# Optimization experiments

Measured on AMD Instinct MI355X. Metric: run time of the kernel, lower is better.

Reference implementation:

```python
import jax, jax.numpy as jnp
import numpy as np

EMB_DIM = 1024
N_HEADS = 16
HEAD_DIM = EMB_DIM // N_HEADS


def setup_inputs() -> dict:
    key = jax.random.key(0)
    ks = jax.random.split(key, 6)
    B, T, C = 2, 2048, EMB_DIM
    s = 1.0 / np.sqrt(C)
    return {
        "x": jax.random.normal(ks[0], (B, T, C), dtype=jnp.float32),
        "W_query": jax.random.normal(ks[1], (C, C), dtype=jnp.float32) * s,
        "W_key": jax.random.normal(ks[2], (C, C), dtype=jnp.float32) * s,
        "W_value": jax.random.normal(ks[3], (C, C), dtype=jnp.float32) * s,
        "W_out": jax.random.normal(ks[4], (C, C), dtype=jnp.float32) * s,
        "b_out": jax.random.normal(ks[5], (C,), dtype=jnp.float32) * 0.01,
    }


def reference(x, W_query, W_key, W_value, W_out, b_out):
    # x: [B, T, C]. Linear weights stored as [in, out] (transposed torch layout).
    B, T, C = x.shape
    H, D = N_HEADS, HEAD_DIM

    def split_heads(t):  # [B,T,C] -> [B,H,T,D]
        return t.reshape(B, T, H, D).transpose(0, 2, 1, 3)

    q = split_heads(x @ W_query)
    k = split_heads(x @ W_key)
    v = split_heads(x @ W_value)

    scale = 1.0 / jnp.sqrt(jnp.asarray(D, dtype=x.dtype))
    att = jnp.einsum("bhqd,bhkd->bhqk", q, k) * scale  # [B,H,T,T]
    causal = jnp.tril(jnp.ones((T, T), dtype=bool))
    att = jnp.where(causal[None, None], att, jnp.asarray(-jnp.inf, dtype=att.dtype))
    att = jax.nn.softmax(att, axis=-1)
    # dropout is identity in eval / drop_rate=0
    y = jnp.einsum("bhqk,bhkd->bhqd", att, v)  # [B,H,T,D]
    y = y.transpose(0, 2, 1, 3).reshape(B, T, C)
    return y @ W_out + b_out
```

## Files before the change

### kernel.cpp

```cpp
#include <hip/hip_runtime.h>
#include <hip/hip_bf16.h>
#include <math.h>

#define Bsz 2
#define Tsz 2048
#define Csz 1024
#define Hsz 16
#define Dsz 64

typedef __attribute__((ext_vector_type(8))) short frag8;
typedef __attribute__((ext_vector_type(4))) float f4;
typedef __attribute__((ext_vector_type(8))) unsigned short us8;

static __device__ __forceinline__ unsigned short f2bf(float f) {
  union { __hip_bfloat16 h; unsigned short u; } c;
  c.h = __float2bfloat16(f);
  return c.u;
}

#define GLDS16(g, l)                                                        \
  __builtin_amdgcn_global_load_lds(                                         \
      (const __attribute__((address_space(1))) void*)(g),                   \
      (__attribute__((address_space(3))) void*)(l), 16, 0, 0)

__global__ __launch_bounds__(256) void cast_x(const float* __restrict__ x,
                                              unsigned short* __restrict__ xb) {
  const int i = (blockIdx.x * 256 + threadIdx.x) * 8;
  const float4 a = *(const float4*)(x + i);
  const float4 b = *(const float4*)(x + i + 4);
  us8 v;
  v[0] = f2bf(a.x); v[1] = f2bf(a.y); v[2] = f2bf(a.z); v[3] = f2bf(a.w);
  v[4] = f2bf(b.x); v[5] = f2bf(b.y); v[6] = f2bf(b.z); v[7] = f2bf(b.w);
  *(us8*)(xb + i) = v;
}

__global__ __launch_bounds__(256) void transpose_cast(
    const float* __restrict__ s0, const float* __restrict__ s1,
    const float* __restrict__ s2, const float* __restrict__ s3,
    unsigned short* __restrict__ d0, unsigned short* __restrict__ d1,
    unsigned short* __restrict__ d2, unsigned short* __restrict__ d3) {
  __shared__ float Ls[64][65];
  const int mat = blockIdx.x >> 8;
  const int tile = blockIdx.x & 255;
  const float* src = mat == 0 ? s0 : mat == 1 ? s1 : mat == 2 ? s2 : s3;
  unsigned short* dst = mat == 0 ? d0 : mat == 1 ? d1 : mat == 2 ? d2 : d3;
  const int tr0 = (tile >> 4) << 6, tc0 = (tile & 15) << 6;
  const int t = threadIdx.x;
  const int lr = t >> 4, lc = (t & 15) << 2;
#pragma unroll
  for (int j = 0; j < 4; ++j) {
    const float4 v = *(const float4*)(src + (size_t)(tr0 + lr + j * 16) * 1024 + tc0 + lc);
    Ls[lr + j * 16][lc + 0] = v.x;
    Ls[lr + j * 16][lc + 1] = v.y;
    Ls[lr + j * 16][lc + 2] = v.z;
    Ls[lr + j * 16][lc + 3] = v.w;
  }
  __syncthreads();
#pragma unroll
  for (int j = 0; j < 4; ++j) {
    ushort4 v;
    v.x = f2bf(Ls[lc + 0][lr + j * 16]);
    v.y = f2bf(Ls[lc + 1][lr + j * 16]);
    v.z = f2bf(Ls[lc + 2][lr + j * 16]);
    v.w = f2bf(Ls[lc + 3][lr + j * 16]);
    *(ushort4*)(dst + (size_t)(tc0 + lr + j * 16) * 1024 + tr0 + lc) = v;
  }
}

template <int MODE>
__global__ __launch_bounds__(256) void mm_bt(
    const unsigned short* __restrict__ A, const unsigned short* __restrict__ Bt,
    const float* __restrict__ bias, unsigned short* __restrict__ O0,
    unsigned short* __restrict__ O1, float* __restrict__ Of) {
  __shared__ __align__(16) unsigned short As[128 * 32];
  __shared__ __align__(16) unsigned short Bs[128 * 32];
  const int K = 1024;
  const int tid = threadIdx.x;
  const int wave = tid >> 6, lane = tid & 63;
  const int quad = lane >> 4, l16 = lane & 15;
  const int wm = wave >> 1, wn = wave & 1;
  const int row0 = blockIdx.y << 7, col0 = blockIdx.x << 7;

  const int sr = lane >> 2, sg = lane & 3;
  const int rA0 = wave * 32 + sr;
  const int g0 = sg ^ ((rA0 >> 1) & 3);
  const unsigned short* gA0 = A + (size_t)(row0 + rA0) * K + (g0 << 3);
  const unsigned short* gA1 = gA0 + (size_t)16 * K;
  const unsigned short* gB0 = Bt + (size_t)(col0 + rA0) * K + (g0 << 3);
  const unsigned short* gB1 = gB0 + (size_t)16 * K;
  unsigned short* lA0 = &As[(wave * 32) * 32];
  unsigned short* lA1 = &As[(wave * 32 + 16) * 32];
  unsigned short* lB0 = &Bs[(wave * 32) * 32];
  unsigned short* lB1 = &Bs[(wave * 32 + 16) * 32];

  f4 acc[4][4];
#pragma unroll
  for (int i = 0; i < 4; ++i)
#pragma unroll
    for (int j = 0; j < 4; ++j) acc[i][j] = (f4){0.f, 0.f, 0.f, 0.f};

  for (int kk = 0; kk < K; kk += 32) {
    __syncthreads();
    GLDS16(gA0 + kk, lA0);
    GLDS16(gA1 + kk, lA1);
    GLDS16(gB0 + kk, lB0);
    GLDS16(gB1 + kk, lB1);
    __syncthreads();

    frag8 af[4], bf[4];
#pragma unroll
    for (int mt = 0; mt < 4; ++mt) {
      const int r = wm * 64 + mt * 16 + l16;
      af[mt] = *(const frag8*)&As[r * 32 + ((quad ^ ((r >> 1) & 3)) << 3)];
    }
#pragma unroll
    for (int nt = 0; nt < 4; ++nt) {
      const int n = wn * 64 + nt * 16 + l16;
      bf[nt] = *(const frag8*)&Bs[n * 32 + ((quad ^ ((n >> 1) & 3)) << 3)];
    }
#pragma unroll
    for (int mt = 0; mt < 4; ++mt)
#pragma unroll
      for (int nt = 0; nt < 4; ++nt)
        acc[mt][nt] = __builtin_amdgcn_mfma_f32_16x16x32_bf16(af[mt], bf[nt], acc[mt][nt], 0, 0, 0);
  }

  if (MODE == 0) {
    const bool isK = (col0 >= 1024);
    unsigned short* dst = isK ? O1 : O0;
    const float sc = isK ? 1.0f : 0.125f;
#pragma unroll
    for (int mt = 0; mt < 4; ++mt)
#pragma unroll
      for (int nt = 0; nt < 4; ++nt) {
        const int m = row0 + wm * 64 + mt * 16 + quad * 4;
        const int n = (col0 & 1023) + wn * 64 + nt * 16 + l16;
        const int b = m >> 11, h = n >> 6, d = n & 63;
#pragma unroll
        for (int r = 0; r < 4; ++r) {
          const int tk = (m + r) & (Tsz - 1);
          dst[(((size_t)b * Hsz + h) * Tsz + tk) * Dsz + d] = f2bf(acc[mt][nt][r] * sc);
        }
      }
  } else if (MODE == 1) {
#pragma unroll
    for (int mt = 0; mt < 4; ++mt)
#pragma unroll
      for (int nt = 0; nt < 4; ++nt) {
        const int ch = row0 + wm * 64 + mt * 16 + quad * 4;
        const int tok = col0 + wn * 64 + nt * 16 + l16;
        const int b = tok >> 11, tk = tok & (Tsz - 1);
#pragma unroll
        for (int r = 0; r < 4; ++r) {
          const int h = (ch + r) >> 6, d = (ch + r) & 63;
          O0[(((size_t)b * Hsz + h) * Dsz + d) * Tsz + tk] = f2bf(acc[mt][nt][r]);
        }
      }
  } else {
#pragma unroll
    for (int mt = 0; mt < 4; ++mt)
#pragma unroll
      for (int nt = 0; nt < 4; ++nt) {
        const int m = row0 + wm * 64 + mt * 16 + quad * 4;
        const int n = col0 + wn * 64 + nt * 16 + l16;
        const float bv = bias[n];
#pragma unroll
        for (int r = 0; r < 4; ++r)
          Of[(size_t)(m + r) * Csz + n] = acc[mt][nt][r] + bv;
      }
  }
}

#define PST 40
__global__ __launch_bounds__(256) void attn_mfma(
    const unsigned short* __restrict__ Qb,
    const unsigned short* __restrict__ Kb,
    const unsigned short* __restrict__ VTb,
    unsigned short* __restrict__ Y) {
  __shared__ __align__(16) unsigned short Pbuf[4][32 * PST];
  const int wave = threadIdx.x >> 6;
  const int lane = threadIdx.x & 63;
  const int quad = lane >> 4;
  const int l16 = lane & 15;

  const int bh = blockIdx.x >> 4;
  int qt = blockIdx.x & 15;
  if (bh >= 16) qt = 15 - qt;

  const int qbase = qt * 128 + wave * 32;

  const unsigned short* Qh = Qb + (size_t)bh * Tsz * Dsz;
  const unsigned short* Kh = Kb + (size_t)bh * Tsz * Dsz;
  const unsigned short* Vh = VTb + (size_t)bh * Dsz * Tsz;

  frag8 qf[2][2];
#pragma unroll
  for (int m = 0; m < 2; ++m)
#pragma unroll
    for (int ks = 0; ks < 2; ++ks)
      qf[m][ks] = *(const frag8*)(Qh + (size_t)(qbase + m * 16 + l16) * Dsz + ks * 32 + quad * 8);

  f4 o[2][4];
  float lsum[2][4];
#pragma unroll
  for (int m = 0; m < 2; ++m) {
#pragma unroll
    for (int nt = 0; nt < 4; ++nt) o[m][nt] = (f4){0.f, 0.f, 0.f, 0.f};
#pragma unroll
    for (int r = 0; r < 4; ++r) lsum[m][r] = 0.f;
  }

  unsigned short* Pw = &Pbuf[wave][0];
  const f4 zf = (f4){0.f, 0.f, 0.f, 0.f};

  const int kend = qbase + 32;
  for (int k0 = 0; k0 < kend; k0 += 32) {
    frag8 kf[2][2];
#pragma unroll
    for (int n = 0; n < 2; ++n)
#pragma unroll
      for (int ks = 0; ks < 2; ++ks)
        kf[n][ks] = *(const frag8*)(Kh + (size_t)(k0 + n * 16 + l16) * Dsz + ks * 32 + quad * 8);
    frag8 vf[4];
#pragma unroll
    for (int nt = 0; nt < 4; ++nt)
      vf[nt] = *(const frag8*)(Vh + (size_t)(nt * 16 + l16) * Tsz + k0 + quad * 8);

    f4 s[2][2];
#pragma unroll
    for (int m = 0; m < 2; ++m)
#pragma unroll
      for (int n = 0; n < 2; ++n) {
        f4 a = __builtin_amdgcn_mfma_f32_16x16x32_bf16(qf[m][0], kf[n][0], zf, 0, 0, 0);
        s[m][n] = __builtin_amdgcn_mfma_f32_16x16x32_bf16(qf[m][1], kf[n][1], a, 0, 0, 0);
      }

#pragma unroll
    for (int m = 0; m < 2; ++m) {
      const int qr0 = qbase + m * 16 + quad * 4;
#pragma unroll
      for (int n = 0; n < 2; ++n) {
        const int kc = k0 + n * 16 + l16;
#pragma unroll
        for (int r = 0; r < 4; ++r) {
          const float sv = (kc <= qr0 + r) ? s[m][n][r] : -INFINITY;
          const float p = __expf(sv);
          lsum[m][r] += p;
          Pw[(m * 16 + quad * 4 + r) * PST + n * 16 + l16] = f2bf(p);
        }
      }
    }

    frag8 pf[2];
#pragma unroll
    for (int m = 0; m < 2; ++m)
      pf[m] = *(const frag8*)(&Pw[(m * 16 + l16) * PST + quad * 8]);

#pragma unroll
    for (int m = 0; m < 2; ++m)
#pragma unroll
      for (int nt = 0; nt < 4; ++nt)
        o[m][nt] = __builtin_amdgcn_mfma_f32_16x16x32_bf16(pf[m], vf[nt], o[m][nt], 0, 0, 0);
  }

#pragma unroll
  for (int off = 1; off < 16; off <<= 1)
#pragma unroll
    for (int m = 0; m < 2; ++m)
#pragma unroll
      for (int r = 0; r < 4; ++r)
        lsum[m][r] += __shfl_xor(lsum[m][r], off);

  const int b = bh >> 4, h = bh & 15;
#pragma unroll
  for (int m = 0; m < 2; ++m) {
#pragma unroll
    for (int r = 0; r < 4; ++r) {
      const float inv = 1.f / lsum[m][r];
      const int trow = qbase + m * 16 + quad * 4 + r;
      unsigned short* yp = Y + ((size_t)b * Tsz + trow) * Csz + h * 64 + l16;
#pragma unroll
      for (int nt = 0; nt < 4; ++nt)
        yp[nt * 16] = f2bf(o[m][nt][r] * inv);
    }
  }
}

extern "C" void kernel_launch(void* const* d_in, const int* in_sizes, int n_in,
                              void* d_out, int out_size, void* d_ws, size_t ws_size,
                              hipStream_t stream) {
  const float* x  = (const float*)d_in[0];
  const float* Wq = (const float*)d_in[1];
  const float* Wk = (const float*)d_in[2];
  const float* Wv = (const float*)d_in[3];
  const float* Wo = (const float*)d_in[4];
  const float* bo = (const float*)d_in[5];

  const size_t NTOK = (size_t)Bsz * Tsz;
  const size_t NEL = NTOK * Csz;
  unsigned short* xb   = (unsigned short*)d_ws;
  unsigned short* WqkT = xb + NEL;
  unsigned short* WvT  = WqkT + 2 * Csz * Csz;
  unsigned short* WoT  = WvT + Csz * Csz;
  unsigned short* Qb   = WoT + Csz * Csz;
  unsigned short* Kb   = Qb + NEL;
  unsigned short* VTb  = Kb + NEL;
  unsigned short* Yb   = VTb + NEL;

  cast_x<<<NEL / 2048, 256, 0, stream>>>(x, xb);
  transpose_cast<<<1024, 256, 0, stream>>>(Wq, Wk, Wv, Wo,
                                           WqkT, WqkT + Csz * Csz, WvT, WoT);

  mm_bt<0><<<dim3(16, 32), 256, 0, stream>>>(xb, WqkT, nullptr, Qb, Kb, nullptr);
  mm_bt<1><<<dim3(32, 8), 256, 0, stream>>>(WvT, xb, nullptr, VTb, nullptr, nullptr);

  attn_mfma<<<Bsz * Hsz * (Tsz / 128), 256, 0, stream>>>(Qb, Kb, VTb, Yb);

  mm_bt<2><<<dim3(8, 32), 256, 0, stream>>>(Yb, WoT, bo, nullptr, nullptr, (float*)d_out);
}
```

Measured before the change: 220.4 us.

## Fuse QKV projection into one GEMM and stage K/V tiles through LDS in attention

The V projection now runs inside the Q/K GEMM launch as a third column range, and writes transposed V with vectorized stores, which removes one kernel launch. The attention kernel now uses 64-query blocks with 16 queries per wave. All four waves share K and V chunks that are double-buffered into swizzled LDS via global_load_lds, instead of each wave reading them from global memory separately. The change also transposes the QK^T MFMA, skips masking on chunks that lie fully below the diagonal, and raises launch_bounds occupancy. In exchange it adds block-wide syncs per chunk and smaller per-wave tiles.

```diff
diff --git a/kernel.cpp b/kernel.cpp
--- a/kernel.cpp
+++ b/kernel.cpp
@@ -71,7 +71,8 @@
 __global__ __launch_bounds__(256) void mm_bt(
     const unsigned short* __restrict__ A, const unsigned short* __restrict__ Bt,
     const float* __restrict__ bias, unsigned short* __restrict__ O0,
-    unsigned short* __restrict__ O1, float* __restrict__ Of) {
+    unsigned short* __restrict__ O1, unsigned short* __restrict__ O2,
+    float* __restrict__ Of) {
   __shared__ __align__(16) unsigned short As[128 * 32];
   __shared__ __align__(16) unsigned short Bs[128 * 32];
   const int K = 1024;
@@ -126,36 +127,38 @@
   }
 
   if (MODE == 0) {
-    const bool isK = (col0 >= 1024);
-    unsigned short* dst = isK ? O1 : O0;
-    const float sc = isK ? 1.0f : 0.125f;
-#pragma unroll
-    for (int mt = 0; mt < 4; ++mt)
-#pragma unroll
-      for (int nt = 0; nt < 4; ++nt) {
-        const int m = row0 + wm * 64 + mt * 16 + quad * 4;
-        const int n = (col0 & 1023) + wn * 64 + nt * 16 + l16;
-        const int b = m >> 11, h = n >> 6, d = n & 63;
-#pragma unroll
-        for (int r = 0; r < 4; ++r) {
-          const int tk = (m + r) & (Tsz - 1);
-          dst[(((size_t)b * Hsz + h) * Tsz + tk) * Dsz + d] = f2bf(acc[mt][nt][r] * sc);
-        }
-      }
-  } else if (MODE == 1) {
-#pragma unroll
-    for (int mt = 0; mt < 4; ++mt)
-#pragma unroll
-      for (int nt = 0; nt < 4; ++nt) {
-        const int ch = row0 + wm * 64 + mt * 16 + quad * 4;
-        const int tok = col0 + wn * 64 + nt * 16 + l16;
-        const int b = tok >> 11, tk = tok & (Tsz - 1);
-#pragma unroll
-        for (int r = 0; r < 4; ++r) {
-          const int h = (ch + r) >> 6, d = (ch + r) & 63;
-          O0[(((size_t)b * Hsz + h) * Dsz + d) * Tsz + tk] = f2bf(acc[mt][nt][r]);
-        }
-      }
+    if (col0 < 2048) {
+      const bool isK = (col0 >= 1024);
+      unsigned short* dst = isK ? O1 : O0;
+      const float sc = isK ? 1.0f : 0.125f;
+#pragma unroll
+      for (int mt = 0; mt < 4; ++mt)
+#pragma unroll
+        for (int nt = 0; nt < 4; ++nt) {
+          const int m = row0 + wm * 64 + mt * 16 + quad * 4;
+          const int n = (col0 & 1023) + wn * 64 + nt * 16 + l16;
+          const int b = m >> 11, h = n >> 6, d = n & 63;
+#pragma unroll
+          for (int r = 0; r < 4; ++r) {
+            const int tk = (m + r) & (Tsz - 1);
+            dst[(((size_t)b * Hsz + h) * Tsz + tk) * Dsz + d] = f2bf(acc[mt][nt][r] * sc);
+          }
+        }
+    } else {
+#pragma unroll
+      for (int mt = 0; mt < 4; ++mt)
+#pragma unroll
+        for (int nt = 0; nt < 4; ++nt) {
+          const int tok = row0 + wm * 64 + mt * 16 + quad * 4;
+          const int ch = (col0 - 2048) + wn * 64 + nt * 16 + l16;
+          const int b = tok >> 11, tk = tok & (Tsz - 1);
+          const int h = ch >> 6, d = ch & 63;
+          ushort4 v;
+          v.x = f2bf(acc[mt][nt][0]); v.y = f2bf(acc[mt][nt][1]);
+          v.z = f2bf(acc[mt][nt][2]); v.w = f2bf(acc[mt][nt][3]);
+          *(ushort4*)&O2[(((size_t)b * Hsz + h) * Dsz + d) * Tsz + tk] = v;
+        }
+    }
   } else {
 #pragma unroll
     for (int mt = 0; mt < 4; ++mt)
@@ -172,117 +175,128 @@
 }
 
 #define PST 40
-__global__ __launch_bounds__(256) void attn_mfma(
+__global__ __launch_bounds__(256, 4) void attn_mfma(
     const unsigned short* __restrict__ Qb,
     const unsigned short* __restrict__ Kb,
     const unsigned short* __restrict__ VTb,
     unsigned short* __restrict__ Y) {
-  __shared__ __align__(16) unsigned short Pbuf[4][32 * PST];
-  const int wave = threadIdx.x >> 6;
-  const int lane = threadIdx.x & 63;
-  const int quad = lane >> 4;
-  const int l16 = lane & 15;
-
-  const int bh = blockIdx.x >> 4;
-  int qt = blockIdx.x & 15;
-  if (bh >= 16) qt = 15 - qt;
-
-  const int qbase = qt * 128 + wave * 32;
+  __shared__ __align__(16) unsigned short Ks[2][2048];
+  __shared__ __align__(16) unsigned short Vs[2][2048];
+  __shared__ __align__(16) unsigned short Pb[4][16 * PST];
+
+  const int tid = threadIdx.x;
+  const int wave = tid >> 6, lane = tid & 63;
+  const int quad = lane >> 4, l16 = lane & 15;
+
+  const int bh = blockIdx.x >> 5;
+  int qt = blockIdx.x & 31;
+  if (bh >= 16) qt = 31 - qt;
+  const int qb_w = (qt << 6) + wave * 16;
 
   const unsigned short* Qh = Qb + (size_t)bh * Tsz * Dsz;
   const unsigned short* Kh = Kb + (size_t)bh * Tsz * Dsz;
   const unsigned short* Vh = VTb + (size_t)bh * Dsz * Tsz;
 
-  frag8 qf[2][2];
-#pragma unroll
-  for (int m = 0; m < 2; ++m)
-#pragma unroll
-    for (int ks = 0; ks < 2; ++ks)
-      qf[m][ks] = *(const frag8*)(Qh + (size_t)(qbase + m * 16 + l16) * Dsz + ks * 32 + quad * 8);
-
-  f4 o[2][4];
-  float lsum[2][4];
-#pragma unroll
-  for (int m = 0; m < 2; ++m) {
-#pragma unroll
-    for (int nt = 0; nt < 4; ++nt) o[m][nt] = (f4){0.f, 0.f, 0.f, 0.f};
-#pragma unroll
-    for (int r = 0; r < 4; ++r) lsum[m][r] = 0.f;
-  }
-
-  unsigned short* Pw = &Pbuf[wave][0];
+  const int kkey = tid >> 3, kc = tid & 7;
+  const int vd = tid >> 2, vc = tid & 3;
+  const unsigned short* gK = Kh + (size_t)kkey * Dsz + ((kc ^ (kkey & 7)) << 3);
+  const unsigned short* gV = Vh + (size_t)vd * Tsz + ((vc ^ ((vd + (vd >> 2)) & 3)) << 3);
+
+  frag8 qf[2];
+  qf[0] = *(const frag8*)(Qh + (size_t)(qb_w + l16) * Dsz + quad * 8);
+  qf[1] = *(const frag8*)(Qh + (size_t)(qb_w + l16) * Dsz + 32 + quad * 8);
+
+  f4 o[4];
+  o[0] = o[1] = o[2] = o[3] = (f4){0.f, 0.f, 0.f, 0.f};
+  float lsum = 0.f;
   const f4 zf = (f4){0.f, 0.f, 0.f, 0.f};
-
-  const int kend = qbase + 32;
-  for (int k0 = 0; k0 < kend; k0 += 32) {
-    frag8 kf[2][2];
-#pragma unroll
-    for (int n = 0; n < 2; ++n)
-#pragma unroll
-      for (int ks = 0; ks < 2; ++ks)
-        kf[n][ks] = *(const frag8*)(Kh + (size_t)(k0 + n * 16 + l16) * Dsz + ks * 32 + quad * 8);
-    frag8 vf[4];
+  unsigned short* Pw = &Pb[wave][0];
+  const int fl = (l16 + (l16 >> 2)) & 3;
+  const int kend_w = qb_w + 16;
+  const int nch = 2 * qt + 2;
+
+  GLDS16(gK, &Ks[0][wave * 512]);
+  GLDS16(gV, &Vs[0][wave * 512]);
+  GLDS16(gK + 32 * Dsz, &Ks[1][wave * 512]);
+  GLDS16(gV + 32, &Vs[1][wave * 512]);
+  __syncthreads();
+
+  for (int i = 0; i < nch; ++i) {
+    const int k0 = i << 5;
+    const int bsel = i & 1;
+    if (k0 < kend_w) {
+      frag8 kf[2][2], vf[4];
+#pragma unroll
+      for (int n = 0; n < 2; ++n)
+#pragma unroll
+        for (int ks = 0; ks < 2; ++ks)
+          kf[n][ks] = *(const frag8*)&Ks[bsel][(n * 16 + l16) * 64 + (((ks * 4 + quad) ^ (l16 & 7)) << 3)];
+#pragma unroll
+      for (int nt = 0; nt < 4; ++nt)
+        vf[nt] = *(const frag8*)&Vs[bsel][(nt * 16 + l16) * 32 + ((quad ^ fl) << 3)];
+
+      f4 st[2];
+#pragma unroll
+      for (int n = 0; n < 2; ++n) {
+        f4 a = __builtin_amdgcn_mfma_f32_16x16x32_bf16(kf[n][0], qf[0], zf, 0, 0, 0);
+        st[n] = __builtin_amdgcn_mfma_f32_16x16x32_bf16(kf[n][1], qf[1], a, 0, 0, 0);
+      }
+
+      const bool domask = (k0 + 31 > qb_w);
+#pragma unroll
+      for (int n = 0; n < 2; ++n) {
+        const int key0 = k0 + n * 16 + quad * 4;
+        ushort4 pk;
+        float p0, p1, p2, p3;
+        {
+          float sv = st[n][0];
+          if (domask && (key0 + 0 > qb_w + l16)) sv = -INFINITY;
+          p0 = __expf(sv);
+        }
+        {
+          float sv = st[n][1];
+          if (domask && (key0 + 1 > qb_w + l16)) sv = -INFINITY;
+          p1 = __expf(sv);
+        }
+        {
+          float sv = st[n][2];
+          if (domask && (key0 + 2 > qb_w + l16)) sv = -INFINITY;
+          p2 = __expf(sv);
+        }
+        {
+          float sv = st[n][3];
+          if (domask && (key0 + 3 > qb_w + l16)) sv = -INFINITY;
+          p3 = __expf(sv);
+        }
+        lsum += (p0 + p1) + (p2 + p3);
+        pk.x = f2bf(p0); pk.y = f2bf(p1); pk.z = f2bf(p2); pk.w = f2bf(p3);
+        *(ushort4*)&Pw[l16 * PST + n * 16 + quad * 4] = pk;
+      }
+
+      const frag8 pf = *(const frag8*)&Pw[l16 * PST + quad * 8];
+#pragma unroll
+      for (int nt = 0; nt < 4; ++nt)
+        o[nt] = __builtin_amdgcn_mfma_f32_16x16x32_bf16(pf, vf[nt], o[nt], 0, 0, 0);
+    }
+    __syncthreads();
+    if (i + 2 < nch) {
+      GLDS16(gK + (size_t)(k0 + 64) * Dsz, &Ks[bsel][wave * 512]);
+      GLDS16(gV + (k0 + 64), &Vs[bsel][wave * 512]);
+    }
+  }
+
+  lsum += __shfl_xor(lsum, 16);
+  lsum += __shfl_xor(lsum, 32);
+
+  const int b = bh >> 4, h = bh & 15;
+#pragma unroll
+  for (int r = 0; r < 4; ++r) {
+    const float inv = 1.f / __shfl(lsum, quad * 4 + r);
+    const int t = qb_w + quad * 4 + r;
+    unsigned short* yp = Y + ((size_t)b * Tsz + t) * Csz + h * 64 + l16;
 #pragma unroll
     for (int nt = 0; nt < 4; ++nt)
-      vf[nt] = *(const frag8*)(Vh + (size_t)(nt * 16 + l16) * Tsz + k0 + quad * 8);
-
-    f4 s[2][2];
-#pragma unroll
-    for (int m = 0; m < 2; ++m)
-#pragma unroll
-      for (int n = 0; n < 2; ++n) {
-        f4 a = __builtin_amdgcn_mfma_f32_16x16x32_bf16(qf[m][0], kf[n][0], zf, 0, 0, 0);
-        s[m][n] = __builtin_amdgcn_mfma_f32_16x16x32_bf16(qf[m][1], kf[n][1], a, 0, 0, 0);
-      }
-
-#pragma unroll
-    for (int m = 0; m < 2; ++m) {
-      const int qr0 = qbase + m * 16 + quad * 4;
-#pragma unroll
-      for (int n = 0; n < 2; ++n) {
-        const int kc = k0 + n * 16 + l16;
-#pragma unroll
-        for (int r = 0; r < 4; ++r) {
-          const float sv = (kc <= qr0 + r) ? s[m][n][r] : -INFINITY;
-          const float p = __expf(sv);
-          lsum[m][r] += p;
-          Pw[(m * 16 + quad * 4 + r) * PST + n * 16 + l16] = f2bf(p);
-        }
-      }
-    }
-
-    frag8 pf[2];
-#pragma unroll
-    for (int m = 0; m < 2; ++m)
-      pf[m] = *(const frag8*)(&Pw[(m * 16 + l16) * PST + quad * 8]);
-
-#pragma unroll
-    for (int m = 0; m < 2; ++m)
-#pragma unroll
-      for (int nt = 0; nt < 4; ++nt)
-        o[m][nt] = __builtin_amdgcn_mfma_f32_16x16x32_bf16(pf[m], vf[nt], o[m][nt], 0, 0, 0);
-  }
-
-#pragma unroll
-  for (int off = 1; off < 16; off <<= 1)
-#pragma unroll
-    for (int m = 0; m < 2; ++m)
-#pragma unroll
-      for (int r = 0; r < 4; ++r)
-        lsum[m][r] += __shfl_xor(lsum[m][r], off);
-
-  const int b = bh >> 4, h = bh & 15;
-#pragma unroll
-  for (int m = 0; m < 2; ++m) {
-#pragma unroll
-    for (int r = 0; r < 4; ++r) {
-      const float inv = 1.f / lsum[m][r];
-      const int trow = qbase + m * 16 + quad * 4 + r;
-      unsigned short* yp = Y + ((size_t)b * Tsz + trow) * Csz + h * 64 + l16;
-#pragma unroll
-      for (int nt = 0; nt < 4; ++nt)
-        yp[nt * 16] = f2bf(o[m][nt][r] * inv);
-    }
+      yp[nt * 16] = f2bf(o[nt][r] * inv);
   }
 }
 
@@ -296,25 +310,24 @@
   const float* Wo = (const float*)d_in[4];
   const float* bo = (const float*)d_in[5];
 
-  const size_t NTOK = (size_t)Bsz * Tsz;
-  const size_t NEL = NTOK * Csz;
-  unsigned short* xb   = (unsigned short*)d_ws;
-  unsigned short* WqkT = xb + NEL;
-  unsigned short* WvT  = WqkT + 2 * Csz * Csz;
-  unsigned short* WoT  = WvT + Csz * Csz;
-  unsigned short* Qb   = WoT + Csz * Csz;
-  unsigned short* Kb   = Qb + NEL;
-  unsigned short* VTb  = Kb + NEL;
-  unsigned short* Yb   = VTb + NEL;
+  const size_t NEL = (size_t)Bsz * Tsz * Csz;
+  const size_t WSZ = (size_t)Csz * Csz;
+  unsigned short* xb  = (unsigned short*)d_ws;
+  unsigned short* WT  = xb + NEL;
+  unsigned short* WoT = WT + 3 * WSZ;
+  unsigned short* Qb  = WoT + WSZ;
+  unsigned short* Kb  = Qb + NEL;
+  unsigned short* VTb = Kb + NEL;
+  unsigned short* Yb  = VTb + NEL;
 
   cast_x<<<NEL / 2048, 256, 0, stream>>>(x, xb);
   transpose_cast<<<1024, 256, 0, stream>>>(Wq, Wk, Wv, Wo,
-                                           WqkT, WqkT + Csz * Csz, WvT, WoT);
-
-  mm_bt<0><<<dim3(16, 32), 256, 0, stream>>>(xb, WqkT, nullptr, Qb, Kb, nullptr);
-  mm_bt<1><<<dim3(32, 8), 256, 0, stream>>>(WvT, xb, nullptr, VTb, nullptr, nullptr);
-
-  attn_mfma<<<Bsz * Hsz * (Tsz / 128), 256, 0, stream>>>(Qb, Kb, VTb, Yb);
-
-  mm_bt<2><<<dim3(8, 32), 256, 0, stream>>>(Yb, WoT, bo, nullptr, nullptr, (float*)d_out);
-}
+                                           WT, WT + WSZ, WT + 2 * WSZ, WoT);
+
+  mm_bt<0><<<dim3(24, 32), 256, 0, stream>>>(xb, WT, nullptr, Qb, Kb, VTb, nullptr);
+
+  attn_mfma<<<Bsz * Hsz * (Tsz / 64), 256, 0, stream>>>(Qb, Kb, VTb, Yb);
+
+  mm_bt<2><<<dim3(8, 32), 256, 0, stream>>>(Yb, WoT, bo, nullptr, nullptr, nullptr,
+                                            (float*)d_out);
+}
```

Result: faster. 196.9 us (-10.7%).
